# Kernel optimization log

Hardware: AMD Instinct MI355X
Metric: run time of the kernel (lower is better)

The kernel has to match this reference:

```python
import jax, jax.numpy as jnp
import numpy as np


def setup_inputs() -> dict:
    key = jax.random.key(0)
    k1, k2, k3 = jax.random.split(key, 3)
    M, C, N, K, L = 4, 2, 512, 16000, 16
    mixture_w = jax.random.normal(k1, (M, N, K), dtype=jnp.float32)
    est_mask = jax.random.uniform(k2, (M, C, N, K), dtype=jnp.float32)
    W = jax.random.normal(k3, (L, N), dtype=jnp.float32) * (1.0 / np.sqrt(N))
    return {"mixture_w": mixture_w, "est_mask": est_mask, "W": W}


def reference(mixture_w, est_mask, W):
    # mixture_w: [M, N, K]; est_mask: [M, C, N, K]; W: [L, N] (torch Linear weight)
    L = W.shape[0]
    hop = L // 2
    source_w = mixture_w[:, None] * est_mask            # [M, C, N, K]
    frames = jnp.einsum('mcnk,ln->mckl', source_w, W)   # [M, C, K, L]
    M, C, K, Lf = frames.shape
    T = (K - 1) * hop + Lf
    # overlap-and-add: frame k writes to samples [k*hop, k*hop+L)
    idx = (jnp.arange(K)[:, None] * hop + jnp.arange(Lf)[None, :]).reshape(-1)
    est_source = jnp.zeros((M, C, T), frames.dtype).at[:, :, idx].add(
        frames.reshape(M, C, K * Lf))
    return est_source
```

## Files before the change

### kernel.cpp

```cpp
#include <hip/hip_runtime.h>


#define M_   4
#define C_   2
#define N_   512
#define K_   16000
#define L_   16
#define HOP  8
#define T_   ((K_ - 1) * HOP + L_)
#define BK   64
#define NSEG 4
#define NPW  (N_ / NSEG)
#define NB   (K_ / BK)
#define WS_TAIL_OFF (M_ * C_ * NB * 8)

__global__ __launch_bounds__(256, 4)
void decoder_kernel(const float* __restrict__ mix,
                    const float* __restrict__ mask,
                    const float* __restrict__ Wg,
                    float* __restrict__ out,
                    float* __restrict__ ws) {
    __shared__ float lds[8192];

    const int tid  = threadIdx.x;
    const int lane = tid & 63;
    const int w    = tid >> 6;
    const int m    = blockIdx.x / NB;
    const int bb   = blockIdx.x % NB;
    const int k0   = bb * BK;

    for (int i = tid; i < L_ * N_; i += 256) lds[i] = Wg[i];
    __syncthreads();

    float acc[32];
    #pragma unroll
    for (int i = 0; i < 32; ++i) acc[i] = 0.f;

    const int n0w = w * NPW;
    const float* pm = mix  + (size_t)m * N_ * K_ + (size_t)n0w * K_ + (k0 + lane);
    const float* p0 = mask + (size_t)(m * C_) * N_ * K_ + (size_t)n0w * K_ + (k0 + lane);
    const float* p1 = p0 + (size_t)N_ * K_;

    #pragma unroll 2
    for (int ch = 0; ch < NPW / 4; ++ch) {
        float mv[4], a0[4], a1[4];
        #pragma unroll
        for (int j = 0; j < 4; ++j) {
            mv[j] = pm[(size_t)j * K_];
            a0[j] = p0[(size_t)j * K_];
            a1[j] = p1[(size_t)j * K_];
        }
        float s0[4], s1[4];
        #pragma unroll
        for (int j = 0; j < 4; ++j) { s0[j] = mv[j] * a0[j]; s1[j] = mv[j] * a1[j]; }

        const int nbase = n0w + ch * 4;
        #pragma unroll
        for (int l = 0; l < L_; ++l) {
            const float4 w4 = *(const float4*)&lds[l * N_ + nbase];
            acc[l]      = fmaf(s0[0], w4.x, acc[l]);
            acc[l]      = fmaf(s0[1], w4.y, acc[l]);
            acc[l]      = fmaf(s0[2], w4.z, acc[l]);
            acc[l]      = fmaf(s0[3], w4.w, acc[l]);
            acc[16 + l] = fmaf(s1[0], w4.x, acc[16 + l]);
            acc[16 + l] = fmaf(s1[1], w4.y, acc[16 + l]);
            acc[16 + l] = fmaf(s1[2], w4.z, acc[16 + l]);
            acc[16 + l] = fmaf(s1[3], w4.w, acc[16 + l]);
        }
        pm += (size_t)4 * K_;
        p0 += (size_t)4 * K_;
        p1 += (size_t)4 * K_;
    }

    __syncthreads();
    if (w > 0) {
        float* rb = &lds[(w - 1) * 2304 + lane * 36];
        #pragma unroll
        for (int i = 0; i < 8; ++i)
            *(float4*)&rb[i * 4] =
                make_float4(acc[i*4], acc[i*4+1], acc[i*4+2], acc[i*4+3]);
    }
    __syncthreads();

    if (w == 0) {
        #pragma unroll
        for (int r = 0; r < 3; ++r) {
            const float* rb = &lds[r * 2304 + lane * 36];
            #pragma unroll
            for (int i = 0; i < 8; ++i) {
                const float4 v = *(const float4*)&rb[i * 4];
                acc[i*4]     += v.x;
                acc[i*4 + 1] += v.y;
                acc[i*4 + 2] += v.z;
                acc[i*4 + 3] += v.w;
            }
        }

        #pragma unroll
        for (int c = 0; c < C_; ++c) {
            float* ob = out + (size_t)(m * C_ + c) * T_ + (size_t)(k0 + lane) * HOP;
            float cmb[8];
            #pragma unroll
            for (int j = 0; j < 8; ++j) {
                const float pv = __shfl_up(acc[c * 16 + 8 + j], 1);
                cmb[j] = acc[c * 16 + j] + pv;
            }
            if (lane == 0) {
                float* hb = ws + (size_t)((m * C_ + c) * NB + bb) * 8;
                *(float4*)&hb[0] = make_float4(acc[c*16+0], acc[c*16+1], acc[c*16+2], acc[c*16+3]);
                *(float4*)&hb[4] = make_float4(acc[c*16+4], acc[c*16+5], acc[c*16+6], acc[c*16+7]);
            } else {
                *(float4*)&ob[0] = make_float4(cmb[0], cmb[1], cmb[2], cmb[3]);
                *(float4*)&ob[4] = make_float4(cmb[4], cmb[5], cmb[6], cmb[7]);
            }
            if (lane == 63) {
                float* tb = ws + WS_TAIL_OFF + (size_t)((m * C_ + c) * NB + bb) * 8;
                *(float4*)&tb[0] = make_float4(acc[c*16+8],  acc[c*16+9],  acc[c*16+10], acc[c*16+11]);
                *(float4*)&tb[4] = make_float4(acc[c*16+12], acc[c*16+13], acc[c*16+14], acc[c*16+15]);
            }
        }
    }
}

__global__ __launch_bounds__(256)
void boundary_kernel(const float* __restrict__ ws, float* __restrict__ out) {
    const int id = blockIdx.x * 256 + threadIdx.x;
    const int total = M_ * C_ * NB * 8;
    if (id >= total) return;
    const int j  = id & 7;
    const int bb = (id >> 3) % NB;
    const int mc = (id >> 3) / NB;
    float v = ws[(size_t)(mc * NB + bb) * 8 + j];
    if (bb > 0) v += ws[WS_TAIL_OFF + (size_t)(mc * NB + bb - 1) * 8 + j];
    out[(size_t)mc * T_ + (size_t)bb * (BK * HOP) + j] = v;
    if (bb == NB - 1) {
        out[(size_t)mc * T_ + (size_t)K_ * HOP + j] =
            ws[WS_TAIL_OFF + (size_t)(mc * NB + bb) * 8 + j];
    }
}

extern "C" void kernel_launch(void* const* d_in, const int* in_sizes, int n_in,
                              void* d_out, int out_size, void* d_ws, size_t ws_size,
                              hipStream_t stream) {
    const float* mix  = (const float*)d_in[0];
    const float* mask = (const float*)d_in[1];
    const float* Wg   = (const float*)d_in[2];
    float* out = (float*)d_out;
    float* ws  = (float*)d_ws;

    decoder_kernel<<<dim3(M_ * NB), dim3(256), 0, stream>>>(mix, mask, Wg, out, ws);
    boundary_kernel<<<dim3((M_ * C_ * NB * 8 + 255) / 256), dim3(256), 0, stream>>>(ws, out);
}
```

Measured before the change: 97.47 us.

## Process two adjacent frames per lane with float2 loads and BK=128

Each lane now computes two consecutive frames (even and odd), loading mixture and mask as float2 and reusing each LDS weight float4 for twice as many FMAs. The block K tile doubles to 128, halving the grid and the per-block W staging into LDS. The cross-wave reduction is split per channel to fit the larger accumulators in the LDS scratch. The cost is double the accumulator registers (64) and a lower occupancy target in launch bounds, which may reduce memory latency hiding in this bandwidth-bound kernel.

```diff
diff --git a/kernel.cpp b/kernel.cpp
--- a/kernel.cpp
+++ b/kernel.cpp
@@ -8,13 +8,13 @@
 #define L_   16
 #define HOP  8
 #define T_   ((K_ - 1) * HOP + L_)
-#define BK   64
+#define BK   128
 #define NSEG 4
 #define NPW  (N_ / NSEG)
 #define NB   (K_ / BK)
 #define WS_TAIL_OFF (M_ * C_ * NB * 8)
 
-__global__ __launch_bounds__(256, 4)
+__global__ __launch_bounds__(256, 2)
 void decoder_kernel(const float* __restrict__ mix,
                     const float* __restrict__ mask,
                     const float* __restrict__ Wg,
@@ -32,91 +32,109 @@
     for (int i = tid; i < L_ * N_; i += 256) lds[i] = Wg[i];
     __syncthreads();
 
-    float acc[32];
+    float accE[32], accO[32];
     #pragma unroll
-    for (int i = 0; i < 32; ++i) acc[i] = 0.f;
+    for (int i = 0; i < 32; ++i) { accE[i] = 0.f; accO[i] = 0.f; }
 
     const int n0w = w * NPW;
-    const float* pm = mix  + (size_t)m * N_ * K_ + (size_t)n0w * K_ + (k0 + lane);
-    const float* p0 = mask + (size_t)(m * C_) * N_ * K_ + (size_t)n0w * K_ + (k0 + lane);
+    const int kk  = k0 + 2 * lane;
+    const float* pm = mix  + (size_t)m * N_ * K_ + (size_t)n0w * K_ + kk;
+    const float* p0 = mask + (size_t)(m * C_) * N_ * K_ + (size_t)n0w * K_ + kk;
     const float* p1 = p0 + (size_t)N_ * K_;
 
     #pragma unroll 2
     for (int ch = 0; ch < NPW / 4; ++ch) {
-        float mv[4], a0[4], a1[4];
+        float2 mv[4], a0[4], a1[4];
         #pragma unroll
         for (int j = 0; j < 4; ++j) {
-            mv[j] = pm[(size_t)j * K_];
-            a0[j] = p0[(size_t)j * K_];
-            a1[j] = p1[(size_t)j * K_];
+            mv[j] = *(const float2*)&pm[(size_t)j * K_];
+            a0[j] = *(const float2*)&p0[(size_t)j * K_];
+            a1[j] = *(const float2*)&p1[(size_t)j * K_];
         }
-        float s0[4], s1[4];
+        float s0e[4], s0o[4], s1e[4], s1o[4];
         #pragma unroll
-        for (int j = 0; j < 4; ++j) { s0[j] = mv[j] * a0[j]; s1[j] = mv[j] * a1[j]; }
-
+        for (int j = 0; j < 4; ++j) {
+            s0e[j] = mv[j].x * a0[j].x;  s0o[j] = mv[j].y * a0[j].y;
+            s1e[j] = mv[j].x * a1[j].x;  s1o[j] = mv[j].y * a1[j].y;
+        }
         const int nbase = n0w + ch * 4;
         #pragma unroll
         for (int l = 0; l < L_; ++l) {
             const float4 w4 = *(const float4*)&lds[l * N_ + nbase];
-            acc[l]      = fmaf(s0[0], w4.x, acc[l]);
-            acc[l]      = fmaf(s0[1], w4.y, acc[l]);
-            acc[l]      = fmaf(s0[2], w4.z, acc[l]);
-            acc[l]      = fmaf(s0[3], w4.w, acc[l]);
-            acc[16 + l] = fmaf(s1[0], w4.x, acc[16 + l]);
-            acc[16 + l] = fmaf(s1[1], w4.y, acc[16 + l]);
-            acc[16 + l] = fmaf(s1[2], w4.z, acc[16 + l]);
-            acc[16 + l] = fmaf(s1[3], w4.w, acc[16 + l]);
+            const float wv[4] = { w4.x, w4.y, w4.z, w4.w };
+            #pragma unroll
+            for (int j = 0; j < 4; ++j) {
+                accE[l]      = fmaf(s0e[j], wv[j], accE[l]);
+                accE[16 + l] = fmaf(s1e[j], wv[j], accE[16 + l]);
+                accO[l]      = fmaf(s0o[j], wv[j], accO[l]);
+                accO[16 + l] = fmaf(s1o[j], wv[j], accO[16 + l]);
+            }
         }
         pm += (size_t)4 * K_;
         p0 += (size_t)4 * K_;
         p1 += (size_t)4 * K_;
     }
 
-    __syncthreads();
-    if (w > 0) {
-        float* rb = &lds[(w - 1) * 2304 + lane * 36];
-        #pragma unroll
-        for (int i = 0; i < 8; ++i)
-            *(float4*)&rb[i * 4] =
-                make_float4(acc[i*4], acc[i*4+1], acc[i*4+2], acc[i*4+3]);
+    #pragma unroll
+    for (int c = 0; c < C_; ++c) {
+        __syncthreads();
+        if (w > 0) {
+            float* rb = &lds[(w - 1) * 2304 + lane * 36];
+            #pragma unroll
+            for (int i = 0; i < 4; ++i)
+                *(float4*)&rb[i * 4] = make_float4(accE[c*16+i*4], accE[c*16+i*4+1],
+                                                   accE[c*16+i*4+2], accE[c*16+i*4+3]);
+            #pragma unroll
+            for (int i = 0; i < 4; ++i)
+                *(float4*)&rb[16 + i * 4] = make_float4(accO[c*16+i*4], accO[c*16+i*4+1],
+                                                        accO[c*16+i*4+2], accO[c*16+i*4+3]);
+        }
+        __syncthreads();
+        if (w == 0) {
+            #pragma unroll
+            for (int r = 0; r < 3; ++r) {
+                const float* rb = &lds[r * 2304 + lane * 36];
+                #pragma unroll
+                for (int i = 0; i < 4; ++i) {
+                    const float4 v = *(const float4*)&rb[i * 4];
+                    accE[c*16+i*4]   += v.x;  accE[c*16+i*4+1] += v.y;
+                    accE[c*16+i*4+2] += v.z;  accE[c*16+i*4+3] += v.w;
+                }
+                #pragma unroll
+                for (int i = 0; i < 4; ++i) {
+                    const float4 v = *(const float4*)&rb[16 + i * 4];
+                    accO[c*16+i*4]   += v.x;  accO[c*16+i*4+1] += v.y;
+                    accO[c*16+i*4+2] += v.z;  accO[c*16+i*4+3] += v.w;
+                }
+            }
+        }
     }
-    __syncthreads();
 
     if (w == 0) {
         #pragma unroll
-        for (int r = 0; r < 3; ++r) {
-            const float* rb = &lds[r * 2304 + lane * 36];
-            #pragma unroll
-            for (int i = 0; i < 8; ++i) {
-                const float4 v = *(const float4*)&rb[i * 4];
-                acc[i*4]     += v.x;
-                acc[i*4 + 1] += v.y;
-                acc[i*4 + 2] += v.z;
-                acc[i*4 + 3] += v.w;
-            }
-        }
-
-        #pragma unroll
         for (int c = 0; c < C_; ++c) {
-            float* ob = out + (size_t)(m * C_ + c) * T_ + (size_t)(k0 + lane) * HOP;
-            float cmb[8];
+            float* ob = out + (size_t)(m * C_ + c) * T_ + (size_t)kk * HOP;
+            float cmbE[8], cmbO[8];
             #pragma unroll
             for (int j = 0; j < 8; ++j) {
-                const float pv = __shfl_up(acc[c * 16 + 8 + j], 1);
-                cmb[j] = acc[c * 16 + j] + pv;
+                const float pv = __shfl_up(accO[c * 16 + 8 + j], 1);
+                cmbE[j] = accE[c * 16 + j] + pv;
+                cmbO[j] = accO[c * 16 + j] + accE[c * 16 + 8 + j];
             }
             if (lane == 0) {
                 float* hb = ws + (size_t)((m * C_ + c) * NB + bb) * 8;
-                *(float4*)&hb[0] = make_float4(acc[c*16+0], acc[c*16+1], acc[c*16+2], acc[c*16+3]);
-                *(float4*)&hb[4] = make_float4(acc[c*16+4], acc[c*16+5], acc[c*16+6], acc[c*16+7]);
+                *(float4*)&hb[0] = make_float4(accE[c*16+0], accE[c*16+1], accE[c*16+2], accE[c*16+3]);
+                *(float4*)&hb[4] = make_float4(accE[c*16+4], accE[c*16+5], accE[c*16+6], accE[c*16+7]);
             } else {
-                *(float4*)&ob[0] = make_float4(cmb[0], cmb[1], cmb[2], cmb[3]);
-                *(float4*)&ob[4] = make_float4(cmb[4], cmb[5], cmb[6], cmb[7]);
+                *(float4*)&ob[0] = make_float4(cmbE[0], cmbE[1], cmbE[2], cmbE[3]);
+                *(float4*)&ob[4] = make_float4(cmbE[4], cmbE[5], cmbE[6], cmbE[7]);
             }
+            *(float4*)&ob[8]  = make_float4(cmbO[0], cmbO[1], cmbO[2], cmbO[3]);
+            *(float4*)&ob[12] = make_float4(cmbO[4], cmbO[5], cmbO[6], cmbO[7]);
             if (lane == 63) {
                 float* tb = ws + WS_TAIL_OFF + (size_t)((m * C_ + c) * NB + bb) * 8;
-                *(float4*)&tb[0] = make_float4(acc[c*16+8],  acc[c*16+9],  acc[c*16+10], acc[c*16+11]);
-                *(float4*)&tb[4] = make_float4(acc[c*16+12], acc[c*16+13], acc[c*16+14], acc[c*16+15]);
+                *(float4*)&tb[0] = make_float4(accO[c*16+8],  accO[c*16+9],  accO[c*16+10], accO[c*16+11]);
+                *(float4*)&tb[4] = make_float4(accO[c*16+12], accO[c*16+13], accO[c*16+14], accO[c*16+15]);
             }
         }
     }
```

New measurement: 119.3 us. 1.22x slower.
